# Kernel tuning notes

Measured on AMD Instinct MI355X. Metric: run time of the kernel, lower is better.

The kernel has to match this reference:

```python
import jax, jax.numpy as jnp
import numpy as np
from jax import lax

# --- static config (mirrors cfg / init args) ---
B, T, F_IN = 4, 1024, 80      # batch, time steps, mel bins (80 -> freq collapses to 1)
C_EMB = 512                   # cfg.dim_embed
C0 = C_EMB // 2               # first_conv_filters (non-tcn branch)
HEADS, K = 8, 7               # num_heads, NA kernel_size (dilation=1)
D_HEAD = C_EMB // HEADS
MLP = 4 * C_EMB               # mlp_ratio=4
EPS = 1e-5                    # layer_norm_eps


def setup_inputs() -> dict:
    key = jax.random.key(0)
    ks = jax.random.split(key, 16)
    rn = lambda k, s, sc=0.02: jax.random.normal(k, s, dtype=jnp.float32) * sc
    z = lambda *s: jnp.zeros(s, dtype=jnp.float32)
    o = lambda *s: jnp.ones(s, dtype=jnp.float32)
    return {
        "x": jax.random.normal(ks[0], (B, 1, T, F_IN), dtype=jnp.float32),
        # conv embedding stack (OIHW)
        "conv0_w": rn(ks[1], (C0, 1, 3, 3), 0.1), "conv0_b": z(C0),
        "conv1_w": rn(ks[2], (C_EMB, C0, 1, 12), 0.02), "conv1_b": z(C_EMB),
        "conv2_w": rn(ks[3], (C_EMB, C_EMB, 3, 3), 0.02), "conv2_b": z(C_EMB),
        "emb_ln_g": o(C_EMB), "emb_ln_b": z(C_EMB),
        # neighborhood attention (linear weights stored [in,out]; apply as x @ W + b)
        "q_w": rn(ks[4], (C_EMB, C_EMB)), "q_b": z(C_EMB),
        "k_w": rn(ks[5], (C_EMB, C_EMB)), "k_b": z(C_EMB),
        "v_w": rn(ks[6], (C_EMB, C_EMB)), "v_b": z(C_EMB),
        "rpb": rn(ks[7], (HEADS, 2 * K - 1)),
        "attn_out_w": rn(ks[8], (C_EMB, C_EMB)), "attn_out_b": z(C_EMB),
        "ln1_g": o(C_EMB), "ln1_b": z(C_EMB),
        "ln2_g": o(C_EMB), "ln2_b": z(C_EMB),
        "mlp1_w": rn(ks[9], (C_EMB, MLP)), "mlp1_b": z(MLP),
        "mlp2_w": rn(ks[10], (MLP, C_EMB)), "mlp2_b": z(C_EMB),
    }


def _layer_norm(x, g, b):
    m = jnp.mean(x, axis=-1, keepdims=True)
    v = jnp.mean(jnp.square(x - m), axis=-1, keepdims=True)
    return (x - m) * lax.rsqrt(v + EPS) * g + b


def _na1d(q, k, v, rpb):
    """1D neighborhood attention (natten1dqkrpb + softmax + natten1dav), dilation=1.
    q,k,v: [B,H,T,D]; rpb: [H,2K-1]. Returns [B,H,T,D]."""
    Bq, H, Tq, D = q.shape
    ni = jnp.clip(jnp.arange(Tq) - K // 2, 0, Tq - K)        # window start per query
    idx = ni[:, None] + jnp.arange(K)                         # [T,K] key positions
    k_win = k[:, :, idx]                                      # [B,H,T,K,D]
    v_win = v[:, :, idx]                                      # [B,H,T,K,D]
    scores = jnp.einsum('bhtd,bhtkd->bhtk', q, k_win)
    rel = idx - jnp.arange(Tq)[:, None] + (K - 1)             # [T,K] in [0,2K-2]
    scores = scores + rpb[:, rel][None]                       # + [1,H,T,K]
    probs = jax.nn.softmax(scores, axis=-1)
    return jnp.einsum('bhtk,bhtkd->bhtd', probs, v_win)


def _forward(x, conv0_w, conv0_b, conv1_w, conv1_b, conv2_w, conv2_b,
             emb_ln_g, emb_ln_b, q_w, q_b, k_w, k_b, v_w, v_b, rpb,
             attn_out_w, attn_out_b, ln1_g, ln1_b, ln2_g, ln2_b,
             mlp1_w, mlp1_b, mlp2_w, mlp2_b):
    conv = lambda h, w, b, pad: lax.conv_general_dilated(
        h, w, (1, 1), pad, dimension_numbers=('NCHW', 'OIHW', 'NCHW')
    ) + b[None, :, None, None]
    pool3 = lambda h: lax.reduce_window(h, -jnp.inf, lax.max,
                                        (1, 1, 1, 3), (1, 1, 1, 3), 'VALID')
    # --- AllInOneEmbeddings (eval: dropouts are no-ops) ---
    h = jax.nn.relu(pool3(conv(x, conv0_w, conv0_b, [(1, 1), (0, 0)])))
    h = jax.nn.relu(pool3(conv(h, conv1_w, conv1_b, [(0, 0), (0, 0)])))
    h = jax.nn.relu(pool3(conv(h, conv2_w, conv2_b, [(1, 1), (0, 0)])))
    h = jnp.transpose(h[..., 0], (0, 2, 1))                   # [B,T,C]
    emb = _layer_norm(h, emb_ln_g, emb_ln_b)
    # --- DinatLayer1d (double_attention=False, drop_path=0) ---
    Bh, Th, Ch = emb.shape
    shortcut = emb
    hs = _layer_norm(emb, ln1_g, ln1_b)
    heads = lambda y: jnp.transpose(y.reshape(Bh, Th, HEADS, D_HEAD), (0, 2, 1, 3))
    q = heads(hs @ q_w + q_b) * (1.0 / jnp.sqrt(jnp.float32(D_HEAD)))
    kk = heads(hs @ k_w + k_b)
    vv = heads(hs @ v_w + v_b)
    ctx = _na1d(q, kk, vv, rpb)                               # [B,H,T,D]
    ctx = jnp.transpose(ctx, (0, 2, 1, 3)).reshape(Bh, Th, Ch)
    attn = ctx @ attn_out_w + attn_out_b                      # NeighborhoodAttentionOutput
    hs = shortcut + attn
    ln = _layer_norm(hs, ln2_g, ln2_b)
    mlp = jax.nn.gelu(ln @ mlp1_w + mlp1_b, approximate=False) @ mlp2_w + mlp2_b
    return hs + mlp


def reference(x, conv0_w, conv0_b, conv1_w, conv1_b, conv2_w, conv2_b,
              emb_ln_g, emb_ln_b, q_w, q_b, k_w, k_b, v_w, v_b, rpb,
              attn_out_w, attn_out_b, ln1_g, ln1_b, ln2_g, ln2_b,
              mlp1_w, mlp1_b, mlp2_w, mlp2_b):
    return _forward(x, conv0_w, conv0_b, conv1_w, conv1_b, conv2_w, conv2_b,
                    emb_ln_g, emb_ln_b, q_w, q_b, k_w, k_b, v_w, v_b, rpb,
                    attn_out_w, attn_out_b, ln1_g, ln1_b, ln2_g, ln2_b,
                    mlp1_w, mlp1_b, mlp2_w, mlp2_b)
```

## Files before the change

### kernel.cpp

```cpp
#include <hip/hip_runtime.h>
#include <hip/hip_bf16.h>
#include <math.h>


typedef __bf16 bf16x8 __attribute__((ext_vector_type(8)));
typedef float f32x4 __attribute__((ext_vector_type(4)));

static __device__ __forceinline__ short f2bf(float f) {
  __hip_bfloat16 h = __float2bfloat16(f);
  return __builtin_bit_cast(short, h);
}

static __device__ __forceinline__ float wave_sum(float v) {
#pragma unroll
  for (int o = 32; o; o >>= 1) v += __shfl_xor(v, o);
  return v;
}

static __device__ __forceinline__ void gld16(const void* g, void* l) {
  __builtin_amdgcn_global_load_lds(
      (const __attribute__((address_space(1))) unsigned int*)g,
      (__attribute__((address_space(3))) unsigned int*)l, 16, 0, 0);
}

__global__ __launch_bounds__(256) void conv0_kernel(
    const float* __restrict__ x, const float* __restrict__ w,
    const float* __restrict__ bias, short* __restrict__ h0) {
  const int b = blockIdx.x >> 10;
  const int t = blockIdx.x & 1023;
  const int c = threadIdx.x;
  __shared__ float xs[3][80];
  for (int i = threadIdx.x; i < 240; i += 256) {
    int dt = i / 80, f = i - dt * 80;
    int tt = t + dt - 1;
    xs[dt][f] = (tt >= 0 && tt < 1024) ? x[(b * 1024 + tt) * 80 + f] : 0.f;
  }
  float wr[9];
#pragma unroll
  for (int i = 0; i < 9; ++i) wr[i] = w[c * 9 + i];
  const float bi = bias[c];
  __syncthreads();
  const int cc = c >> 5, q = (c >> 3) & 3, e = c & 7;
  short* outb = &h0[((size_t)(b * 8 + cc) * 1024 + t) * 896];
  for (int fo = 0; fo < 26; ++fo) {
    float m = -1e30f;
#pragma unroll
    for (int p = 0; p < 3; ++p) {
      const int f = fo * 3 + p;
      float acc = bi;
#pragma unroll
      for (int dt = 0; dt < 3; ++dt)
#pragma unroll
        for (int df = 0; df < 3; ++df)
          acc += xs[dt][f + df] * wr[dt * 3 + df];
      m = fmaxf(m, acc);
    }
    const int row = t * 28 + fo;
    outb[fo * 32 + (q ^ ((row >> 1) & 3)) * 8 + e] = f2bf(fmaxf(m, 0.f));
  }
  if (c < 64) outb[832 + c] = 0;
}

__global__ __launch_bounds__(256) void prep_w1(const float* __restrict__ w,
                                               short* __restrict__ wt) {
  const int co = blockIdx.x;
  __shared__ float ls[3072];
  for (int i = threadIdx.x; i < 3072; i += 256) ls[i] = w[co * 3072 + i];
  __syncthreads();
  const int swz = (co >> 1) & 3;
  for (int i = threadIdx.x; i < 3072; i += 256) {
    const int e = i & 7, q = (i >> 3) & 3, kw = (i >> 5) % 12, cc = i / 384;
    const int ci = cc * 32 + q * 8 + e;
    wt[(((size_t)(cc * 12 + kw) * 512 + co) * 4 + (q ^ swz)) * 8 + e] =
        f2bf(ls[ci * 12 + kw]);
  }
}

__global__ __launch_bounds__(256) void prep_w2(const float* __restrict__ w,
                                               short* __restrict__ wt) {
  const int co = blockIdx.x;
  __shared__ float ls[4608];
  for (int i = threadIdx.x; i < 4608; i += 256) ls[i] = w[co * 4608 + i];
  __syncthreads();
  const int swz = (co >> 1) & 3;
  for (int i = threadIdx.x; i < 4608; i += 256) {
    const int e = i & 7, q = (i >> 3) & 3, p = (i >> 5) % 9, cc = i / 288;
    const int ci = cc * 32 + q * 8 + e;
    wt[(((size_t)(cc * 9 + p) * 512 + co) * 4 + (q ^ swz)) * 8 + e] =
        f2bf(ls[ci * 9 + p]);
  }
}

__global__ void prep_wt(const float* __restrict__ w, short* __restrict__ wt,
                        int K, int N) {
  __shared__ float tile[32][33];
  const int k0 = blockIdx.x * 32, n0 = blockIdx.y * 32;
  const int tx = threadIdx.x, ty = threadIdx.y;
  for (int r = ty; r < 32; r += 8) tile[r][tx] = w[(size_t)(k0 + r) * N + n0 + tx];
  __syncthreads();
  for (int r = ty; r < 32; r += 8) wt[(size_t)(n0 + r) * K + k0 + tx] = f2bf(tile[tx][r]);
}

__global__ __launch_bounds__(256) void zero_h1_edges(short* __restrict__ h1) {
  short* base = h1 + (size_t)blockIdx.x * 164160;
  for (int i = threadIdx.x; i < 160; i += 256) {
    base[i] = 0;
    base[1025 * 160 + i] = 0;
  }
}

__global__ __launch_bounds__(256) void concat3_kernel(
    const float* __restrict__ a, const float* __restrict__ b,
    const float* __restrict__ c, float* __restrict__ o) {
  const int i = blockIdx.x * 256 + threadIdx.x;
  o[i] = i < 512 ? a[i] : (i < 1024 ? b[i - 512] : c[i - 1024]);
}

__global__ __launch_bounds__(256) void conv1_kernel(
    const short* __restrict__ h0, const short* __restrict__ wt1,
    const float* __restrict__ bias, short* __restrict__ h1) {
  const int b = blockIdx.x >> 6;
  const int t0 = (blockIdx.x & 63) * 16;
  const int co0 = blockIdx.y * 128;
  __shared__ short XsF[2][14336];
  __shared__ short AsF[2][4096];
  const int tid = threadIdx.x;
  const int lane = tid & 63;
  const int wid = tid >> 6;
  const int wm = wid >> 1;
  const int wn = wid & 1;
  const int l15 = lane & 15, lg = lane >> 4;

  const f32x4 zf = {0.f, 0.f, 0.f, 0.f};
  f32x4 acc[4][8];
#pragma unroll
  for (int i = 0; i < 4; ++i)
#pragma unroll
    for (int j = 0; j < 8; ++j) acc[i][j] = zf;

  auto stageX = [&](int cc, int buf) {
    const short* xs = h0 + ((size_t)(b * 8 + cc) * 1024 + t0) * 896;
#pragma unroll
    for (int i = 0; i < 7; ++i) {
      const int v = wid * 7 + i;
      gld16(xs + v * 512 + lane * 8, &XsF[buf][v * 512]);
    }
  };
  auto stageA = [&](int cc, int kw, int buf) {
#pragma unroll
    for (int i = 0; i < 2; ++i) {
      const int r = wid * 2 + i;
      gld16(wt1 + ((size_t)((cc * 12 + kw) * 512) + co0) * 32 + r * 512 + lane * 8,
            &AsF[buf][r * 512]);
    }
  };

  stageX(0, 0);
  stageA(0, 0, 0);
  asm volatile("s_waitcnt vmcnt(0)" ::: "memory");
  __builtin_amdgcn_s_barrier();

  for (int s = 0; s < 96; ++s) {
    const int cc = s / 12, kw = s - cc * 12;
    if (s < 95) {
      const int s1 = s + 1;
      const int cc1 = s1 / 12, kw1 = s1 - cc1 * 12;
      stageA(cc1, kw1, s1 & 1);
      if (kw1 == 0) {
        stageX(cc1, cc1 & 1);
        asm volatile("s_waitcnt vmcnt(9)" ::: "memory");
      } else {
        asm volatile("s_waitcnt vmcnt(2)" ::: "memory");
      }
    } else {
      asm volatile("s_waitcnt vmcnt(0)" ::: "memory");
    }
    __builtin_amdgcn_s_barrier();
    const short* Xb = XsF[cc & 1];
    const short* Ab = AsF[s & 1];
    bf16x8 a[4];
#pragma unroll
    for (int sm = 0; sm < 4; ++sm) {
      const int co_l = wm * 64 + sm * 16 + l15;
      a[sm] = *reinterpret_cast<const bf16x8*>(
          &Ab[(co_l * 4 + (lg ^ ((co_l >> 1) & 3))) * 8]);
    }
#pragma unroll
    for (int sn = 0; sn < 8; ++sn) {
      const int row = (wn * 8 + sn) * 28 + l15 + kw;
      bf16x8 bf = *reinterpret_cast<const bf16x8*>(
          &Xb[(row * 4 + (lg ^ ((row >> 1) & 3))) * 8]);
#pragma unroll
      for (int sm = 0; sm < 4; ++sm)
        acc[sm][sn] = __builtin_amdgcn_mfma_f32_16x16x32_bf16(a[sm], bf, acc[sm][sn], 0, 0, 0);
    }
    asm volatile("" ::: "memory");
    __builtin_amdgcn_s_barrier();
  }
  const int basel = lane & 48;
  const int wsrc = (l15 < 5) ? 3 * l15 : 0;
#pragma unroll
  for (int sm = 0; sm < 4; ++sm)
#pragma unroll
    for (int sn = 0; sn < 8; ++sn) {
      const int t = t0 + wn * 8 + sn;
#pragma unroll
      for (int r = 0; r < 4; ++r) {
        float val = acc[sm][sn][r];
        float v0 = __shfl(val, basel + wsrc);
        float v1 = __shfl(val, basel + wsrc + 1);
        float v2 = __shfl(val, basel + wsrc + 2);
        if (l15 < 5) {
          const int co = co0 + wm * 64 + sm * 16 + lg * 4 + r;
          float p = fmaxf(fmaxf(v0, v1), v2) + bias[co];
          const int cc2 = co >> 5, q = (co >> 3) & 3, e = co & 7;
          const int row_g = (t + 1) * 5 + l15;
          h1[((size_t)(b * 16 + cc2) * 1026 + (t + 1)) * 160 + l15 * 32 +
             (q ^ ((row_g >> 1) & 3)) * 8 + e] = f2bf(fmaxf(p, 0.f));
        }
      }
    }
}

__global__ __launch_bounds__(512) void conv2_kernel(
    const short* __restrict__ h1, const short* __restrict__ wt2,
    const float* __restrict__ bias, float* __restrict__ emb_in) {
  const int b = blockIdx.x >> 5;
  const int t0 = (blockIdx.x & 31) * 32;
  const int co0 = blockIdx.y * 128;
  __shared__ __align__(16) short smem2[35840];
  const int tid = threadIdx.x;
  const int lane = tid & 63;
  const int wid = tid >> 6;
  const int wm = wid >> 1;
  const int wn = wid & 1;
  const int l15 = lane & 15, lg = lane >> 4;
  const f32x4 zf = {0.f, 0.f, 0.f, 0.f};
  f32x4 acc[2][3];
#pragma unroll
  for (int i = 0; i < 2; ++i)
#pragma unroll
    for (int j = 0; j < 3; ++j) acc[i][j] = zf;
  int tl[3], dwl[3];
#pragma unroll
  for (int sn = 0; sn < 3; ++sn) {
    const int c = wn * 48 + sn * 16 + l15;
    tl[sn] = c / 3;
    dwl[sn] = c - tl[sn] * 3;
  }

  auto stageX = [&](int cc, int buf) {
    const short* xs = h1 + ((size_t)(b * 16 + cc) * 1026 + t0) * 160;
#pragma unroll
    for (int i = 0; i < 2; ++i) {
      const int v = wid + 8 * i;
      if (v < 11) gld16(xs + v * 512 + lane * 8, &smem2[buf * 5632 + v * 512]);
    }
  };
  auto stageA = [&](int cc, int g, int buf) {
#pragma unroll
    for (int i = 0; i < 3; ++i) {
      const int u = wid * 3 + i;
      const int pl = u >> 3, r = u & 7;
      gld16(wt2 + ((size_t)((cc * 9 + g * 3 + pl) * 512) + co0) * 32 +
                r * 512 + lane * 8,
            &smem2[11264 + buf * 12288 + pl * 4096 + r * 512]);
    }
  };

  stageX(0, 0);
  stageA(0, 0, 0);
  asm volatile("s_waitcnt vmcnt(0)" ::: "memory");
  __builtin_amdgcn_s_barrier();

  for (int s = 0; s < 48; ++s) {
    const int cc = s / 3, g = s - cc * 3;
    if (s < 47) {
      const int s1 = s + 1;
      const int cc1 = s1 / 3, g1 = s1 - cc1 * 3;
      stageA(cc1, g1, s1 & 1);
      if (g1 == 0) {
        stageX(cc1, cc1 & 1);
        if (wid < 3) asm volatile("s_waitcnt vmcnt(5)" ::: "memory");
        else         asm volatile("s_waitcnt vmcnt(4)" ::: "memory");
      } else {
        asm volatile("s_waitcnt vmcnt(3)" ::: "memory");
      }
    } else {
      asm volatile("s_waitcnt vmcnt(0)" ::: "memory");
    }
    __builtin_amdgcn_s_barrier();
    const short* Xb = &smem2[(cc & 1) * 5632];
    const short* Ab = &smem2[11264 + (s & 1) * 12288];
#pragma unroll
    for (int j = 0; j < 3; ++j) {
      bf16x8 a[2];
#pragma unroll
      for (int sm = 0; sm < 2; ++sm) {
        const int co_l = wm * 32 + sm * 16 + l15;
        a[sm] = *reinterpret_cast<const bf16x8*>(
            &Ab[(j * 512 + co_l * 4 + (lg ^ ((co_l >> 1) & 3))) * 8]);
      }
#pragma unroll
      for (int sn = 0; sn < 3; ++sn) {
        const int row = (tl[sn] + g) * 5 + dwl[sn] + j;
        bf16x8 xv = *reinterpret_cast<const bf16x8*>(
            &Xb[(row * 4 + (lg ^ ((row >> 1) & 3))) * 8]);
#pragma unroll
        for (int sm = 0; sm < 2; ++sm)
          acc[sm][sn] = __builtin_amdgcn_mfma_f32_16x16x32_bf16(a[sm], xv, acc[sm][sn], 0, 0, 0);
      }
    }
    asm volatile("" ::: "memory");
    __builtin_amdgcn_s_barrier();
  }
  float(*Ds)[100] = reinterpret_cast<float(*)[100]>(smem2);
#pragma unroll
  for (int sm = 0; sm < 2; ++sm)
#pragma unroll
    for (int sn = 0; sn < 3; ++sn)
#pragma unroll
      for (int r = 0; r < 4; ++r)
        Ds[wm * 32 + sm * 16 + lg * 4 + r][wn * 48 + sn * 16 + l15] = acc[sm][sn][r];
  __syncthreads();
  for (int e = tid; e < 4096; e += 512) {
    const int co = e & 127, tt = e >> 7;
    float m = fmaxf(fmaxf(Ds[co][tt * 3], Ds[co][tt * 3 + 1]), Ds[co][tt * 3 + 2]) + bias[co0 + co];
    emb_in[((size_t)(b * 1024) + t0 + tt) * 512 + co0 + co] = fmaxf(m, 0.f);
  }
}

__global__ __launch_bounds__(256) void ln_double_kernel(
    const float* __restrict__ x, const float* __restrict__ g0,
    const float* __restrict__ b0, const float* __restrict__ g1,
    const float* __restrict__ b1, float* __restrict__ o0, short* __restrict__ o1) {
  const int row = blockIdx.x * 4 + (threadIdx.x >> 6);
  const int lane = threadIdx.x & 63;
  const float* xr = x + (size_t)row * 512;
  float v[8];
#pragma unroll
  for (int j = 0; j < 8; ++j) v[j] = xr[j * 64 + lane];
  float s = 0;
#pragma unroll
  for (int j = 0; j < 8; ++j) s += v[j];
  s = wave_sum(s);
  const float mean = s * (1.f / 512.f);
  float q = 0;
#pragma unroll
  for (int j = 0; j < 8; ++j) { float d = v[j] - mean; q += d * d; }
  q = wave_sum(q);
  const float rs = rsqrtf(q * (1.f / 512.f) + 1e-5f);
#pragma unroll
  for (int j = 0; j < 8; ++j) {
    const int ci = j * 64 + lane;
    float e = (v[j] - mean) * rs * g0[ci] + b0[ci];
    o0[(size_t)row * 512 + ci] = e;
    v[j] = e;
  }
  s = 0;
#pragma unroll
  for (int j = 0; j < 8; ++j) s += v[j];
  s = wave_sum(s);
  const float mean2 = s * (1.f / 512.f);
  q = 0;
#pragma unroll
  for (int j = 0; j < 8; ++j) { float d = v[j] - mean2; q += d * d; }
  q = wave_sum(q);
  const float rs2 = rsqrtf(q * (1.f / 512.f) + 1e-5f);
#pragma unroll
  for (int j = 0; j < 8; ++j) {
    const int ci = j * 64 + lane;
    o1[(size_t)row * 512 + ci] = f2bf((v[j] - mean2) * rs2 * g1[ci] + b1[ci]);
  }
}

__global__ __launch_bounds__(256) void ln_kernel(
    const float* __restrict__ x, const float* __restrict__ g,
    const float* __restrict__ b, short* __restrict__ o) {
  const int row = blockIdx.x * 4 + (threadIdx.x >> 6);
  const int lane = threadIdx.x & 63;
  const float* xr = x + (size_t)row * 512;
  float v[8];
#pragma unroll
  for (int j = 0; j < 8; ++j) v[j] = xr[j * 64 + lane];
  float s = 0;
#pragma unroll
  for (int j = 0; j < 8; ++j) s += v[j];
  s = wave_sum(s);
  const float mean = s * (1.f / 512.f);
  float q = 0;
#pragma unroll
  for (int j = 0; j < 8; ++j) { float d = v[j] - mean; q += d * d; }
  q = wave_sum(q);
  const float rs = rsqrtf(q * (1.f / 512.f) + 1e-5f);
#pragma unroll
  for (int j = 0; j < 8; ++j) {
    const int ci = j * 64 + lane;
    o[(size_t)row * 512 + ci] = f2bf((v[j] - mean) * rs * g[ci] + b[ci]);
  }
}

__global__ __launch_bounds__(256) void na1d_kernel(
    const float* __restrict__ qkv, const float* __restrict__ rpb,
    short* __restrict__ ctx) {
  const int W = blockIdx.x * 4 + (threadIdx.x >> 6);
  const int lane = threadIdx.x & 63;
  const int b = W >> 13, h = (W >> 10) & 7, t = W & 1023;
  int ni = t - 3;
  ni = ni < 0 ? 0 : (ni > 1017 ? 1017 : ni);
  const float qv = qkv[((size_t)(b * 1024) + t) * 1536 + h * 64 + lane];
  const float* kb = qkv + 512 + ((size_t)(b * 1024) + ni) * 1536 + h * 64;
  float s[7];
#pragma unroll
  for (int j = 0; j < 7; ++j) {
    float pd = qv * kb[j * 1536 + lane];
    pd = wave_sum(pd);
    s[j] = pd + rpb[h * 13 + (ni + j - t + 6)];
  }
  float mx = s[0];
#pragma unroll
  for (int j = 1; j < 7; ++j) mx = fmaxf(mx, s[j]);
  float den = 0;
#pragma unroll
  for (int j = 0; j < 7; ++j) { s[j] = expf(s[j] - mx); den += s[j]; }
  const float inv = 1.f / den;
  const float* vb = qkv + 1024 + ((size_t)(b * 1024) + ni) * 1536 + h * 64;
  float o = 0;
#pragma unroll
  for (int j = 0; j < 7; ++j) o += s[j] * vb[j * 1536 + lane];
  ctx[((size_t)(b * 1024) + t) * 512 + h * 64 + lane] = f2bf(o * inv);
}

template <int EPI>
__global__ __launch_bounds__(256) void gemm_bf(
    const short* __restrict__ A, const short* __restrict__ Wt,
    const float* __restrict__ bias, const float* __restrict__ res,
    void* __restrict__ Cv, int K, int N) {
  const int m0 = blockIdx.x * 128, n0 = blockIdx.y * 64;
  __shared__ short Asm[2][8192];
  __shared__ short Bsm[2][4096];
  const int tid = threadIdx.x;
  const int wid = tid >> 6, lane = tid & 63;
  const int wm = wid >> 1, wn = wid & 1;
  const int l15 = lane & 15, lg = lane >> 4;
  const int srow = lane >> 3, su = lane & 7;
  const int ssw = (su ^ srow) << 3;
  const f32x4 zf = {0.f, 0.f, 0.f, 0.f};
  f32x4 acc[4][2];
#pragma unroll
  for (int i = 0; i < 4; ++i) { acc[i][0] = zf; acc[i][1] = zf; }

  auto stage = [&](int k0, int buf) {
#pragma unroll
    for (int i = 0; i < 4; ++i) {
      const int r0 = (wid * 4 + i) * 8;
      gld16(A + (size_t)(m0 + r0 + srow) * K + k0 + ssw, &Asm[buf][r0 * 64]);
    }
#pragma unroll
    for (int i = 0; i < 2; ++i) {
      const int r0 = (wid * 2 + i) * 8;
      gld16(Wt + (size_t)(n0 + r0 + srow) * K + k0 + ssw, &Bsm[buf][r0 * 64]);
    }
  };

  const int S = K >> 6;
  stage(0, 0);
  asm volatile("s_waitcnt vmcnt(0)" ::: "memory");
  __builtin_amdgcn_s_barrier();

  for (int s = 0; s < S; ++s) {
    if (s < S - 1) {
      stage((s + 1) << 6, (s + 1) & 1);
      asm volatile("s_waitcnt vmcnt(6)" ::: "memory");
    } else {
      asm volatile("s_waitcnt vmcnt(0)" ::: "memory");
    }
    __builtin_amdgcn_s_barrier();
    const short* Ab = Asm[s & 1];
    const short* Bb = Bsm[s & 1];
#pragma unroll
    for (int kk = 0; kk < 2; ++kk) {
      const int u = kk * 4 + lg;
      bf16x8 bfr[2];
#pragma unroll
      for (int sn = 0; sn < 2; ++sn) {
        const int rn = wn * 32 + sn * 16 + l15;
        bfr[sn] = *reinterpret_cast<const bf16x8*>(&Bb[rn * 64 + ((u ^ (rn & 7)) << 3)]);
      }
#pragma unroll
      for (int sm = 0; sm < 4; ++sm) {
        const int rm = wm * 64 + sm * 16 + l15;
        bf16x8 a = *reinterpret_cast<const bf16x8*>(&Ab[rm * 64 + ((u ^ (rm & 7)) << 3)]);
#pragma unroll
        for (int sn = 0; sn < 2; ++sn)
          acc[sm][sn] = __builtin_amdgcn_mfma_f32_16x16x32_bf16(a, bfr[sn], acc[sm][sn], 0, 0, 0);
      }
    }
    asm volatile("" ::: "memory");
    __builtin_amdgcn_s_barrier();
  }
#pragma unroll
  for (int sm = 0; sm < 4; ++sm)
#pragma unroll
    for (int sn = 0; sn < 2; ++sn)
#pragma unroll
      for (int r = 0; r < 4; ++r) {
        const int m = m0 + wm * 64 + sm * 16 + lg * 4 + r;
        const int n = n0 + wn * 32 + sn * 16 + l15;
        float val = acc[sm][sn][r] + bias[n];
        if (EPI == 2) {
          val = 0.5f * val * (1.f + erff(val * 0.70710678f));
          ((short*)Cv)[(size_t)m * N + n] = f2bf(val);
        } else {
          if (EPI == 3) val += res[(size_t)m * N + n];
          if (EPI == 4 && n < 512) val *= 0.125f;
          ((float*)Cv)[(size_t)m * N + n] = val;
        }
      }
}

extern "C" void kernel_launch(void* const* d_in, const int* in_sizes, int n_in,
                              void* d_out, int out_size, void* d_ws, size_t ws_size,
                              hipStream_t stream) {
  (void)in_sizes; (void)n_in; (void)out_size;
  const float* x        = (const float*)d_in[0];
  const float* conv0_w  = (const float*)d_in[1];
  const float* conv0_b  = (const float*)d_in[2];
  const float* conv1_w  = (const float*)d_in[3];
  const float* conv1_b  = (const float*)d_in[4];
  const float* conv2_w  = (const float*)d_in[5];
  const float* conv2_b  = (const float*)d_in[6];
  const float* emb_ln_g = (const float*)d_in[7];
  const float* emb_ln_b = (const float*)d_in[8];
  const float* q_w  = (const float*)d_in[9];
  const float* q_b  = (const float*)d_in[10];
  const float* k_w  = (const float*)d_in[11];
  const float* k_b  = (const float*)d_in[12];
  const float* v_w  = (const float*)d_in[13];
  const float* v_b  = (const float*)d_in[14];
  const float* rpb  = (const float*)d_in[15];
  const float* ao_w = (const float*)d_in[16];
  const float* ao_b = (const float*)d_in[17];
  const float* ln1_g = (const float*)d_in[18];
  const float* ln1_b = (const float*)d_in[19];
  const float* ln2_g = (const float*)d_in[20];
  const float* ln2_b = (const float*)d_in[21];
  const float* m1_w = (const float*)d_in[22];
  const float* m1_b = (const float*)d_in[23];
  const float* m2_w = (const float*)d_in[24];
  const float* m2_b = (const float*)d_in[25];

  char* ws = (char*)d_ws;
  size_t off = 0;
  auto alloc = [&](size_t bytes) -> char* {
    char* p = ws + off;
    off += (bytes + 255) & ~(size_t)255;
    return p;
  };
  short* h0   = (short*)alloc(4ull * 8 * 1024 * 896 * 2);
  short* h1   = (short*)alloc(4ull * 16 * 1026 * 160 * 2);
  float* embi = (float*)alloc(4ull * 1024 * 512 * 4);
  float* emb  = (float*)alloc(4ull * 1024 * 512 * 4);
  short* hs1  = (short*)alloc(4ull * 1024 * 512 * 2);
  float* qkv  = (float*)alloc(4ull * 1024 * 1536 * 4);
  short* ctx  = (short*)alloc(4ull * 1024 * 512 * 2);
  float* hs   = (float*)alloc(4ull * 1024 * 512 * 4);
  short* wt1  = (short*)alloc(512ull * 12 * 256 * 2);
  short* wt2  = (short*)alloc(512ull * 9 * 512 * 2);
  short* wtqkv = (short*)alloc(1536ull * 512 * 2);
  short* wtao = (short*)alloc(512ull * 512 * 2);
  short* wtm1 = (short*)alloc(2048ull * 512 * 2);
  short* wtm2 = (short*)alloc(512ull * 2048 * 2);
  float* qkvb = (float*)alloc(1536ull * 4);
  if (ws_size < off) return;
  short* mid  = (short*)h0;
  short* ln2o = (short*)embi;
  float* outp = (float*)d_out;

  prep_w1<<<512, 256, 0, stream>>>(conv1_w, wt1);
  prep_w2<<<512, 256, 0, stream>>>(conv2_w, wt2);
  zero_h1_edges<<<64, 256, 0, stream>>>(h1);
  concat3_kernel<<<6, 256, 0, stream>>>(q_b, k_b, v_b, qkvb);
  dim3 tb(32, 8);
  prep_wt<<<dim3(16, 16), tb, 0, stream>>>(q_w, wtqkv, 512, 512);
  prep_wt<<<dim3(16, 16), tb, 0, stream>>>(k_w, wtqkv + 512 * 512, 512, 512);
  prep_wt<<<dim3(16, 16), tb, 0, stream>>>(v_w, wtqkv + 1024 * 512, 512, 512);
  prep_wt<<<dim3(16, 16), tb, 0, stream>>>(ao_w, wtao, 512, 512);
  prep_wt<<<dim3(16, 64), tb, 0, stream>>>(m1_w, wtm1, 512, 2048);
  prep_wt<<<dim3(64, 16), tb, 0, stream>>>(m2_w, wtm2, 2048, 512);

  conv0_kernel<<<4096, 256, 0, stream>>>(x, conv0_w, conv0_b, h0);
  conv1_kernel<<<dim3(256, 4), 256, 0, stream>>>(h0, wt1, conv1_b, h1);
  conv2_kernel<<<dim3(128, 4), 512, 0, stream>>>(h1, wt2, conv2_b, embi);
  ln_double_kernel<<<1024, 256, 0, stream>>>(embi, emb_ln_g, emb_ln_b, ln1_g, ln1_b, emb, hs1);
  gemm_bf<4><<<dim3(32, 24), 256, 0, stream>>>(hs1, wtqkv, qkvb, nullptr, qkv, 512, 1536);
  na1d_kernel<<<8192, 256, 0, stream>>>(qkv, rpb, ctx);
  gemm_bf<3><<<dim3(32, 8), 256, 0, stream>>>(ctx, wtao, ao_b, emb, hs, 512, 512);
  ln_kernel<<<1024, 256, 0, stream>>>(hs, ln2_g, ln2_b, ln2o);
  gemm_bf<2><<<dim3(32, 32), 256, 0, stream>>>(ln2o, wtm1, m1_b, nullptr, mid, 512, 2048);
  gemm_bf<3><<<dim3(32, 8), 256, 0, stream>>>(mid, wtm2, m2_b, hs, outp, 2048, 512);
}
```

Baseline: 429.5 us.

## Enlarge conv1 tile to 32 time steps with 512 threads, single-buffer X

Conv1 blocks now cover 32 time steps with 8 waves (a 2x4 wave grid) instead of 16 steps with 4 waves. This halves the grid and doubles the reuse of each staged weight tile. The X input is now single-buffered and loaded synchronously between channel chunks instead of being prefetched, which frees LDS for the larger tile. In exchange, the X loads are no longer overlapped with compute at each chunk boundary.

```diff
diff --git a/kernel.cpp b/kernel.cpp
--- a/kernel.cpp
+++ b/kernel.cpp
@@ -116,19 +116,19 @@
   o[i] = i < 512 ? a[i] : (i < 1024 ? b[i - 512] : c[i - 1024]);
 }
 
-__global__ __launch_bounds__(256) void conv1_kernel(
+__global__ __launch_bounds__(512, 4) void conv1_kernel(
     const short* __restrict__ h0, const short* __restrict__ wt1,
     const float* __restrict__ bias, short* __restrict__ h1) {
-  const int b = blockIdx.x >> 6;
-  const int t0 = (blockIdx.x & 63) * 16;
+  const int b = blockIdx.x >> 5;
+  const int t0 = (blockIdx.x & 31) * 32;
   const int co0 = blockIdx.y * 128;
-  __shared__ short XsF[2][14336];
+  __shared__ short Xs[28672];
   __shared__ short AsF[2][4096];
   const int tid = threadIdx.x;
   const int lane = tid & 63;
   const int wid = tid >> 6;
-  const int wm = wid >> 1;
-  const int wn = wid & 1;
+  const int wm = wid >> 2;
+  const int wn = wid & 3;
   const int l15 = lane & 15, lg = lane >> 4;
 
   const f32x4 zf = {0.f, 0.f, 0.f, 0.f};
@@ -138,64 +138,59 @@
 #pragma unroll
     for (int j = 0; j < 8; ++j) acc[i][j] = zf;
 
-  auto stageX = [&](int cc, int buf) {
+  auto stageX = [&](int cc) {
     const short* xs = h0 + ((size_t)(b * 8 + cc) * 1024 + t0) * 896;
 #pragma unroll
     for (int i = 0; i < 7; ++i) {
       const int v = wid * 7 + i;
-      gld16(xs + v * 512 + lane * 8, &XsF[buf][v * 512]);
+      gld16(xs + v * 512 + lane * 8, &Xs[v * 512]);
     }
   };
   auto stageA = [&](int cc, int kw, int buf) {
-#pragma unroll
-    for (int i = 0; i < 2; ++i) {
-      const int r = wid * 2 + i;
-      gld16(wt1 + ((size_t)((cc * 12 + kw) * 512) + co0) * 32 + r * 512 + lane * 8,
-            &AsF[buf][r * 512]);
-    }
+    gld16(wt1 + ((size_t)((cc * 12 + kw) * 512) + co0) * 32 + wid * 512 + lane * 8,
+          &AsF[buf][wid * 512]);
   };
 
-  stageX(0, 0);
+  stageX(0);
   stageA(0, 0, 0);
   asm volatile("s_waitcnt vmcnt(0)" ::: "memory");
   __builtin_amdgcn_s_barrier();
 
-  for (int s = 0; s < 96; ++s) {
-    const int cc = s / 12, kw = s - cc * 12;
-    if (s < 95) {
-      const int s1 = s + 1;
-      const int cc1 = s1 / 12, kw1 = s1 - cc1 * 12;
-      stageA(cc1, kw1, s1 & 1);
-      if (kw1 == 0) {
-        stageX(cc1, cc1 & 1);
-        asm volatile("s_waitcnt vmcnt(9)" ::: "memory");
+  for (int cc = 0; cc < 8; ++cc) {
+    for (int kw = 0; kw < 12; ++kw) {
+      if (kw < 11) {
+        stageA(cc, kw + 1, (kw + 1) & 1);
+        asm volatile("s_waitcnt vmcnt(1)" ::: "memory");
       } else {
-        asm volatile("s_waitcnt vmcnt(2)" ::: "memory");
-      }
-    } else {
+        asm volatile("s_waitcnt vmcnt(0)" ::: "memory");
+      }
+      __builtin_amdgcn_s_barrier();
+      const short* Ab = AsF[kw & 1];
+      bf16x8 a[4];
+#pragma unroll
+      for (int sm = 0; sm < 4; ++sm) {
+        const int co_l = wm * 64 + sm * 16 + l15;
+        a[sm] = *reinterpret_cast<const bf16x8*>(
+            &Ab[(co_l * 4 + (lg ^ ((co_l >> 1) & 3))) * 8]);
+      }
+#pragma unroll
+      for (int sn = 0; sn < 8; ++sn) {
+        const int row = (wn * 8 + sn) * 28 + l15 + kw;
+        bf16x8 bf = *reinterpret_cast<const bf16x8*>(
+            &Xs[(row * 4 + (lg ^ ((row >> 1) & 3))) * 8]);
+#pragma unroll
+        for (int sm = 0; sm < 4; ++sm)
+          acc[sm][sn] = __builtin_amdgcn_mfma_f32_16x16x32_bf16(a[sm], bf, acc[sm][sn], 0, 0, 0);
+      }
+      asm volatile("" ::: "memory");
+      __builtin_amdgcn_s_barrier();
+    }
+    if (cc < 7) {
+      stageX(cc + 1);
+      stageA(cc + 1, 0, 0);
       asm volatile("s_waitcnt vmcnt(0)" ::: "memory");
-    }
-    __builtin_amdgcn_s_barrier();
-    const short* Xb = XsF[cc & 1];
-    const short* Ab = AsF[s & 1];
-    bf16x8 a[4];
-#pragma unroll
-    for (int sm = 0; sm < 4; ++sm) {
-      const int co_l = wm * 64 + sm * 16 + l15;
-      a[sm] = *reinterpret_cast<const bf16x8*>(
-          &Ab[(co_l * 4 + (lg ^ ((co_l >> 1) & 3))) * 8]);
-    }
-#pragma unroll
-    for (int sn = 0; sn < 8; ++sn) {
-      const int row = (wn * 8 + sn) * 28 + l15 + kw;
-      bf16x8 bf = *reinterpret_cast<const bf16x8*>(
-          &Xb[(row * 4 + (lg ^ ((row >> 1) & 3))) * 8]);
-#pragma unroll
-      for (int sm = 0; sm < 4; ++sm)
-        acc[sm][sn] = __builtin_amdgcn_mfma_f32_16x16x32_bf16(a[sm], bf, acc[sm][sn], 0, 0, 0);
-    }
-    asm volatile("" ::: "memory");
-    __builtin_amdgcn_s_barrier();
+      __builtin_amdgcn_s_barrier();
+    }
   }
   const int basel = lane & 48;
   const int wsrc = (l15 < 5) ? 3 * l15 : 0;
@@ -590,7 +585,7 @@
   prep_wt<<<dim3(64, 16), tb, 0, stream>>>(m2_w, wtm2, 2048, 512);
 
   conv0_kernel<<<4096, 256, 0, stream>>>(x, conv0_w, conv0_b, h0);
-  conv1_kernel<<<dim3(256, 4), 256, 0, stream>>>(h0, wt1, conv1_b, h1);
+  conv1_kernel<<<dim3(128, 4), 512, 0, stream>>>(h0, wt1, conv1_b, h1);
   conv2_kernel<<<dim3(128, 4), 512, 0, stream>>>(h1, wt2, conv2_b, embi);
   ln_double_kernel<<<1024, 256, 0, stream>>>(embi, emb_ln_g, emb_ln_b, ln1_g, ln1_b, emb, hs1);
   gemm_bf<4><<<dim3(32, 24), 256, 0, stream>>>(hs1, wtqkv, qkvb, nullptr, qkv, 512, 1536);
```

After: 1.490 ms. 247% more time.
